# Kernel tuning notes

Hardware: AMD Instinct MI355X
Metric: run time of the kernel (lower is better)

Reference implementation:

```python
import jax, jax.numpy as jnp
import numpy as np

NUM_HEADS = 32
NUM_KV_GROUPS = 8


def _rope(x, cos, sin):
    # x: [B, H, S, hd]; cos/sin: [S_max, hd]
    S, hd = x.shape[2], x.shape[3]
    x1, x2 = x[..., : hd // 2], x[..., hd // 2 :]
    rotated = jnp.concatenate((-x2, x1), axis=-1)
    c = cos[:S][None, None]
    s = sin[:S][None, None]
    return (x * c + rotated * s).astype(x.dtype)


def setup_inputs() -> dict:
    key = jax.random.key(0)
    ks = jax.random.split(key, 8)
    B, S, D = 2, 2048, 2048
    H, G = NUM_HEADS, NUM_KV_GROUPS
    hd = D // H
    scale = 1.0 / np.sqrt(D)
    return {
        "inputs": jax.random.normal(ks[0], (B, S, D), jnp.float32),
        "mask": jnp.zeros((S, S), jnp.bool_),  # note: original masked_fill is not in-place -> mask unused
        "cos": jax.random.uniform(ks[1], (S, hd), jnp.float32),
        "sin": jax.random.uniform(ks[2], (S, hd), jnp.float32),
        "Wq": jax.random.normal(ks[3], (D, H * hd), jnp.float32) * scale,
        "Wk": jax.random.normal(ks[4], (D, G * hd), jnp.float32) * scale,
        "Wv": jax.random.normal(ks[5], (D, G * hd), jnp.float32) * scale,
        "Wo": jax.random.normal(ks[6], (H * hd, H * hd), jnp.float32) * scale,
    }


def reference(inputs, mask, cos, sin, Wq, Wk, Wv, Wo):
    B, S, D = inputs.shape
    H, G = NUM_HEADS, NUM_KV_GROUPS
    hd = Wq.shape[1] // H
    group_size = H // G

    q = (inputs @ Wq).reshape(B, S, H, hd).transpose(0, 2, 1, 3)  # [B,H,S,hd]
    k = (inputs @ Wk).reshape(B, S, G, hd).transpose(0, 2, 1, 3)  # [B,G,S,hd]
    v = (inputs @ Wv).reshape(B, S, G, hd).transpose(0, 2, 1, 3)

    q = _rope(q, cos, sin)
    k = _rope(k, cos, sin)

    k = jnp.repeat(k, group_size, axis=1)  # [B,H,S,hd]
    v = jnp.repeat(v, group_size, axis=1)

    scores = jnp.einsum("bhqd,bhkd->bhqk", q, k)
    # NOTE: original uses non-inplace masked_fill whose result is discarded,
    # so faithfully NO mask is applied.
    attn = jax.nn.softmax(scores / jnp.sqrt(jnp.float32(hd)).astype(scores.dtype), axis=-1)
    ctx = jnp.einsum("bhqk,bhkd->bhqd", attn, v)
    ctx = ctx.transpose(0, 2, 1, 3).reshape(B, S, H * hd)
    return ctx @ Wo
```

## Files before the change

kernel.cpp:

```cpp
#include <hip/hip_runtime.h>
#include <stdint.h>

typedef __attribute__((ext_vector_type(8))) short short8;
typedef __attribute__((ext_vector_type(4))) short short4v;
typedef __attribute__((ext_vector_type(4))) float float4v;
typedef __attribute__((ext_vector_type(2))) unsigned uint2v;

__device__ __forceinline__ float bf2f(short s) {
  union { unsigned u; float f; } x;
  x.u = ((unsigned)(unsigned short)s) << 16;
  return x.f;
}
__device__ __forceinline__ short f2bf(float f) {
  union { float f; unsigned u; } x;
  x.f = f;
  unsigned r = x.u + 0x7fffu + ((x.u >> 16) & 1u);
  return (short)(r >> 16);
}
__device__ __forceinline__ float fexp2(float x) {
#if __has_builtin(__builtin_amdgcn_exp2f)
  return __builtin_amdgcn_exp2f(x);
#else
  float r;
  asm("v_exp_f32 %0, %1" : "=v"(r) : "v"(x));
  return r;
#endif
}
__device__ __forceinline__ void glds16(const void* g, void* l) {
  __builtin_amdgcn_global_load_lds(
      (const __attribute__((address_space(1))) void*)g,
      (__attribute__((address_space(3))) void*)l, 16, 0, 0);
}
__device__ __forceinline__ void sbar() {
  __builtin_amdgcn_sched_barrier(0);
  __builtin_amdgcn_s_barrier();
  __builtin_amdgcn_sched_barrier(0);
}

__global__ __launch_bounds__(256) void f32_to_bf16(const float* __restrict__ s,
                                                   short* __restrict__ d) {
  const long i = ((long)blockIdx.x * 256 + threadIdx.x) * 8;
  const float4v a = *(const float4v*)&s[i];
  const float4v b = *(const float4v*)&s[i + 4];
  short8 v;
#pragma unroll
  for (int e = 0; e < 4; ++e) { v[e] = f2bf(a[e]); v[e + 4] = f2bf(b[e]); }
  *(short8*)&d[i] = v;
}

__device__ __forceinline__ void transpose_tile(
    const float* __restrict__ src, short* __restrict__ dst, int R, int C,
    int r0, int c0) {
  __shared__ short t[64 * 72];
  const int tid = threadIdx.x;
#pragma unroll
  for (int r = 0; r < 2; ++r) {
    int c = r * 256 + tid;
    int row = c >> 3, col8 = (c & 7) * 8;
    const float4v a = *(const float4v*)&src[(long)(r0 + row) * C + c0 + col8];
    const float4v b = *(const float4v*)&src[(long)(r0 + row) * C + c0 + col8 + 4];
    short8 v;
#pragma unroll
    for (int e = 0; e < 4; ++e) { v[e] = f2bf(a[e]); v[e + 4] = f2bf(b[e]); }
    *(short8*)&t[row * 72 + col8] = v;
  }
  __syncthreads();
#pragma unroll
  for (int r = 0; r < 2; ++r) {
    int c = r * 256 + tid;
    int orow = c >> 3, ocol8 = (c & 7) * 8;
    short8 w;
#pragma unroll
    for (int e = 0; e < 8; ++e) w[e] = t[(ocol8 + e) * 72 + orow];
    *(short8*)&dst[(long)(c0 + orow) * R + r0 + ocol8] = w;
  }
}

__global__ __launch_bounds__(256) void transpose_f2b(
    const float* __restrict__ src, short* __restrict__ dst, int R, int C) {
  transpose_tile(src, dst, R, C, blockIdx.y * 64, blockIdx.x * 64);
}

__global__ __launch_bounds__(256) void wtrans3(
    const float* __restrict__ Wq, const float* __restrict__ Wk,
    const float* __restrict__ Wv, short* __restrict__ WT) {
  const int z = blockIdx.z;
  const float* src = z == 0 ? Wq : (z == 1 ? Wk : Wv);
  const int C = z == 0 ? 2048 : 512;
  if (blockIdx.x * 64 >= C) return;
  short* dst = WT + (z == 0 ? 0 : (z == 1 ? 2048 * 2048 : 2560 * 2048));
  transpose_tile(src, dst, 2048, C, blockIdx.y * 64, blockIdx.x * 64);
}

__global__ __launch_bounds__(256) void vtrans(const short* __restrict__ Y,
                                              short* __restrict__ Vt,
                                              int ld, int col0) {
  const int bg = blockIdx.y;
  const int b = bg >> 3, gk = bg & 7;
  const int s0 = blockIdx.x * 64;
  __shared__ short t[64 * 72];
  const int tid = threadIdx.x;
#pragma unroll
  for (int r = 0; r < 2; ++r) {
    int c = r * 256 + tid;
    int row = c >> 3, col8 = (c & 7) * 8;
    short8 v = *(const short8*)&Y[(long)(b * 2048 + s0 + row) * ld + col0 + gk * 64 + col8];
    *(short8*)&t[row * 72 + col8] = v;
  }
  __syncthreads();
#pragma unroll
  for (int r = 0; r < 2; ++r) {
    int c = r * 256 + tid;
    int d = c >> 3, s8 = (c & 7) * 8;
    short8 w;
#pragma unroll
    for (int e = 0; e < 8; ++e) w[e] = t[(s8 + e) * 72 + d];
    *(short8*)&Vt[((long)bg * 64 + d) * 2048 + s0 + s8] = w;
  }
}

__global__ __launch_bounds__(256) void rope_kernel(
    const short* __restrict__ Y, const float* __restrict__ cosp,
    const float* __restrict__ sinp, short* __restrict__ out,
    int NH, int lgNH, int ld, int col0, float scale) {
  const long tid = (long)blockIdx.x * 256 + threadIdx.x;
  const int d = (int)(tid & 31);
  const long t1 = tid >> 5;
  const int h = (int)(t1 & (NH - 1));
  const long t2 = t1 >> lgNH;
  const int s = (int)(t2 & 2047);
  const int b = (int)(t2 >> 11);
  const long ib = (long)(b * 2048 + s) * ld + col0 + h * 64 + d;
  const float x1 = bf2f(Y[ib]);
  const float x2 = bf2f(Y[ib + 32]);
  const float c1 = cosp[s * 64 + d];
  const float c2 = cosp[s * 64 + d + 32];
  const float s1 = sinp[s * 64 + d];
  const float s2 = sinp[s * 64 + d + 32];
  const long ob = ((long)(b * NH + h) * 2048 + s) * 64 + d;
  out[ob] = f2bf((x1 * c1 - x2 * s1) * scale);
  out[ob + 32] = f2bf((x2 * c2 + x1 * s2) * scale);
}

template <typename OutT>
__global__ __launch_bounds__(512, 2) void gemm256(
    const short* __restrict__ A, const short* __restrict__ BT,
    OutT* __restrict__ C, int M, int N, int K) {
  (void)M;
  __shared__ short As[2][16384];
  __shared__ short Bs[2][16384];
  const int tid = threadIdx.x;
  const int w = tid >> 6, lane = tid & 63;
  const int g = lane >> 4, lr = lane & 15;
  const int wm = w >> 2, wn = w & 3;
  const int m0 = blockIdx.y << 8, n0 = blockIdx.x << 8;

  const int r0 = tid >> 3;
  const int scol = ((tid & 7) << 3) ^ (((r0 >> 2) & 1) << 4);
  const long aoff = (long)(m0 + r0) * K + scol;
  const long boff = (long)(n0 + r0) * K + scol;

  const int swz = ((lr >> 2) & 1) << 4;
  const int acol0 = (g << 3) ^ swz;
  const int acol1 = (32 + (g << 3)) ^ swz;
  const int abase = (wm * 128 + lr) * 64;
  const int bbase = (wn * 64 + lr) * 64;

  float4v acc[8][4];
#pragma unroll
  for (int i = 0; i < 8; ++i)
#pragma unroll
    for (int j = 0; j < 4; ++j) acc[i][j] = (float4v)0.f;

#define STAGE_A(l, buf, kg)                                          \
  glds16(A + aoff + (long)(l) * 64 * K + (kg),                       \
         &As[(buf)][(l) * 4096 + w * 512])
#define STAGE_B(l, buf, kg)                                          \
  glds16(BT + boff + (long)(l) * 64 * K + (kg),                      \
         &Bs[(buf)][(l) * 4096 + w * 512])

  const int NT = K >> 6;
#pragma unroll
  for (int l = 0; l < 4; ++l) { STAGE_A(l, 0, 0); STAGE_B(l, 0, 0); }
#pragma unroll
  for (int l = 0; l < 4; ++l) { STAGE_A(l, 1, 64); STAGE_B(l, 1, 64); }
  asm volatile("s_waitcnt vmcnt(8)" ::: "memory");
  sbar();

  short8 aR[4][2], bR0[2][2], bR1[2][2];

#define LDA(MH, ASB)                                                       \
  _Pragma("unroll") for (int i = 0; i < 4; ++i) {                          \
    aR[i][0] = *(const short8*)&ASB[abase + ((MH)*4 + i) * 1024 + acol0];  \
    aR[i][1] = *(const short8*)&ASB[abase + ((MH)*4 + i) * 1024 + acol1];  \
  }
#define LDB(NH, BSB, BR)                                                   \
  _Pragma("unroll") for (int j = 0; j < 2; ++j) {                          \
    BR[j][0] = *(const short8*)&BSB[bbase + ((NH)*2 + j) * 1024 + acol0];  \
    BR[j][1] = *(const short8*)&BSB[bbase + ((NH)*2 + j) * 1024 + acol1];  \
  }
#define MMA_Q(MH, NH, BR)                                                  \
  __builtin_amdgcn_s_setprio(1);                                           \
  _Pragma("unroll") for (int kk = 0; kk < 2; ++kk)                         \
  _Pragma("unroll") for (int i = 0; i < 4; ++i)                            \
  _Pragma("unroll") for (int j = 0; j < 2; ++j)                            \
    acc[(MH)*4 + i][(NH)*2 + j] = __builtin_amdgcn_mfma_f32_16x16x32_bf16( \
        aR[i][kk], BR[j][kk], acc[(MH)*4 + i][(NH)*2 + j], 0, 0, 0);       \
  __builtin_amdgcn_s_setprio(0);

  for (int t = 0; t < NT; ++t) {
    const short* const Asb = As[t & 1];
    const short* const Bsb = Bs[t & 1];
    const long kg = (long)(t + 2) << 6;
    const bool pre = (t + 2) < NT;

    LDA(0, Asb);
    LDB(0, Bsb, bR0);
    sbar();
    MMA_Q(0, 0, bR0);
    sbar();
    LDB(1, Bsb, bR1);
    if (pre) { STAGE_A(0, t & 1, kg); STAGE_A(2, t & 1, kg); }
    sbar();
    MMA_Q(0, 1, bR1);
    sbar();
    LDA(1, Asb);
    if (pre) {
      STAGE_B(0, t & 1, kg); STAGE_B(1, t & 1, kg);
      STAGE_B(2, t & 1, kg); STAGE_B(3, t & 1, kg);
    }
    sbar();
    MMA_Q(1, 1, bR1);
    sbar();
    if (pre) { STAGE_A(1, t & 1, kg); STAGE_A(3, t & 1, kg); }
    sbar();
    MMA_Q(1, 0, bR0);
    __builtin_amdgcn_sched_barrier(0);
    if (pre) { asm volatile("s_waitcnt vmcnt(8)" ::: "memory"); }
    else     { asm volatile("s_waitcnt vmcnt(0)" ::: "memory"); }
    sbar();
  }

#pragma unroll
  for (int i = 0; i < 8; ++i)
#pragma unroll
    for (int j = 0; j < 4; ++j)
#pragma unroll
      for (int t4 = 0; t4 < 4; ++t4) {
        const int r = m0 + wm * 128 + i * 16 + g * 4 + t4;
        const int cc = n0 + wn * 64 + j * 16 + lr;
        const float v = acc[i][j][t4];
        if constexpr (sizeof(OutT) == 2)
          C[(long)r * N + cc] = f2bf(v);
        else
          C[(long)r * N + cc] = v;
      }
#undef STAGE_A
#undef STAGE_B
#undef LDA
#undef LDB
#undef MMA_Q
}

__global__ __launch_bounds__(512, 2) void attn_kernel(
    const short* __restrict__ Qr, const short* __restrict__ Kr,
    const short* __restrict__ Vt, short* __restrict__ Ctx) {
  constexpr int S = 2048;
  const int bh = blockIdx.y;
  const int b = bh >> 5, h = bh & 31;
  const int gk = h >> 2;
  const int q0 = blockIdx.x << 7;
  const int tid = threadIdx.x;
  const int w = tid >> 6, lane = tid & 63;
  const int g = lane >> 4, lr = lane & 15;
  const int b8 = lr & 7;
  const int qrow = w * 16 + lr;

  __shared__ short Ks[128 * 64];
  __shared__ short Vs[64 * 128];
  __shared__ short Ps[128 * 128];

  const short* Qb = Qr + (long)(b * 32 + h) * S * 64;
  const short* KbIt = Kr + (long)(b * 8 + gk) * S * 64;
  const short* VbIt = Vt + (long)(b * 8 + gk) * 64 * S;

  const int ko0 = lr * 64 + ((0 + g) ^ b8) * 8;
  const int ko1 = lr * 64 + ((4 + g) ^ b8) * 8;
  const int jv0 = g ^ b8;
  const int vo0 = lr * 128 + jv0 * 8;
  const int vo1 = lr * 128 + (jv0 ^ 4) * 8;
  int pr[4], pw[8];
#pragma unroll
  for (int ks = 0; ks < 4; ++ks) pr[ks] = qrow * 128 + ((4 * ks + g) ^ b8) * 8;
#pragma unroll
  for (int i = 0; i < 8; ++i)
    pw[i] = qrow * 128 + ((2 * i + (g >> 1)) ^ b8) * 8 + (g & 1) * 4;

  long koff[2], voff[2];
#pragma unroll
  for (int r = 0; r < 2; ++r) {
    const int c = r * 512 + w * 64 + lane;
    const int kv = c >> 3, slot = c & 7;
    koff[r] = (long)kv * 64 + (slot ^ (kv & 7)) * 8;
    const int dd = c >> 4, s16 = c & 15;
    voff[r] = (long)dd * S + ((s16 & 8) | ((s16 & 7) ^ (dd & 7))) * 8;
  }

  short8 qf[2];
  qf[0] = *(const short8*)&Qb[(long)(q0 + qrow) * 64 + g * 8];
  qf[1] = *(const short8*)&Qb[(long)(q0 + qrow) * 64 + 32 + g * 8];

  const short8 ones = (short8)(short)0x3F80;
  float4v lacc = (float4v)0.f;
  float4v oacc[4];
#pragma unroll
  for (int di = 0; di < 4; ++di) oacc[di] = (float4v)0.f;

  for (int it = 0; it < 16; ++it) {
#pragma unroll
    for (int r = 0; r < 2; ++r) {
      const int cb = r * 512 + w * 64;
      glds16(KbIt + koff[r], Ks + cb * 8);
      glds16(VbIt + voff[r], Vs + cb * 8);
    }
    __syncthreads();

    float4v sacc[8];
#pragma unroll
    for (int i = 0; i < 8; ++i) sacc[i] = (float4v)0.f;
#pragma unroll
    for (int i = 0; i < 8; ++i) {
      const short8 a0 = *(const short8*)&Ks[ko0 + i * 1024];
      sacc[i] = __builtin_amdgcn_mfma_f32_16x16x32_bf16(a0, qf[0], sacc[i], 0, 0, 0);
    }
#pragma unroll
    for (int i = 0; i < 8; ++i) {
      const short8 a1 = *(const short8*)&Ks[ko1 + i * 1024];
      sacc[i] = __builtin_amdgcn_mfma_f32_16x16x32_bf16(a1, qf[1], sacc[i], 0, 0, 0);
    }

#pragma unroll
    for (int i = 0; i < 8; ++i) {
      union { float f; unsigned u; } a0, a1, a2, a3;
      a0.f = fexp2(sacc[i][0]);
      a1.f = fexp2(sacc[i][1]);
      a2.f = fexp2(sacc[i][2]);
      a3.f = fexp2(sacc[i][3]);
      const unsigned d0 = __builtin_amdgcn_perm(a1.u + 0x8000u, a0.u + 0x8000u, 0x07060302u);
      const unsigned d1 = __builtin_amdgcn_perm(a3.u + 0x8000u, a2.u + 0x8000u, 0x07060302u);
      *(uint2v*)&Ps[pw[i]] = (uint2v){d0, d1};
    }

#pragma unroll
    for (int ks = 0; ks < 4; ++ks) {
      const short8 pf = *(const short8*)&Ps[pr[ks]];
      const int vbase = (ks & 1) ? vo1 : vo0;
      lacc = __builtin_amdgcn_mfma_f32_16x16x32_bf16(ones, pf, lacc, 0, 0, 0);
#pragma unroll
      for (int di = 0; di < 4; ++di) {
        const short8 vf = *(const short8*)&Vs[vbase + di * 2048 + (ks >> 1) * 64];
        oacc[di] = __builtin_amdgcn_mfma_f32_16x16x32_bf16(vf, pf, oacc[di], 0, 0, 0);
      }
    }
    __syncthreads();
    KbIt += 128 * 64;
    VbIt += 128;
  }

  const float inv = 1.f / lacc[0];

  const int q = q0 + qrow;
#pragma unroll
  for (int di = 0; di < 4; ++di) {
    short4v o;
#pragma unroll
    for (int t = 0; t < 4; ++t) o[t] = f2bf(oacc[di][t] * inv);
    *(short4v*)&Ctx[(long)(b * S + q) * 2048 + h * 64 + di * 16 + g * 4] = o;
  }
}

extern "C" void kernel_launch(void* const* d_in, const int* in_sizes, int n_in,
                              void* d_out, int out_size, void* d_ws, size_t ws_size,
                              hipStream_t stream) {
  (void)in_sizes; (void)n_in; (void)out_size; (void)ws_size;
  const float* X    = (const float*)d_in[0];
  const float* cosp = (const float*)d_in[2];
  const float* sinp = (const float*)d_in[3];
  const float* Wq   = (const float*)d_in[4];
  const float* Wk   = (const float*)d_in[5];
  const float* Wv   = (const float*)d_in[6];
  const float* Wo   = (const float*)d_in[7];
  float* out = (float*)d_out;
  char* ws = (char*)d_ws;

  short* Xb = (short*)(ws + 0);
  short* WT = (short*)(ws + 16777216);
  short* Y  = (short*)(ws + 29360128);
  short* Qr = (short*)(ws + 54525952);
  short* Kr = (short*)(ws + 71303168);
  short* Vt = (short*)(ws + 75497472);

  f32_to_bf16<<<4096, 256, 0, stream>>>(X, Xb);
  wtrans3<<<dim3(32, 32, 3), 256, 0, stream>>>(Wq, Wk, Wv, WT);

  gemm256<short><<<dim3(12, 16), 512, 0, stream>>>(Xb, WT, Y, 4096, 3072, 2048);

  transpose_f2b<<<dim3(32, 32), 256, 0, stream>>>(Wo, WT, 2048, 2048);

  rope_kernel<<<16384, 256, 0, stream>>>(Y, cosp, sinp, Qr, 32, 5, 3072, 0, 0.18033688011112043f);
  rope_kernel<<<4096, 256, 0, stream>>>(Y, cosp, sinp, Kr, 8, 3, 3072, 2048, 1.0f);
  vtrans<<<dim3(32, 16), 256, 0, stream>>>(Y, Vt, 3072, 2560);

  attn_kernel<<<dim3(16, 64), 512, 0, stream>>>(Qr, Kr, Vt, Y);

  gemm256<float><<<dim3(8, 16), 512, 0, stream>>>(Y, WT, out, 4096, 2048, 2048);
}
```

Measured before the change: 386.4 us.

## Double-buffer attention K/V tiles and remap GEMM block order with wider swizzle

The attention kernel switches from 128-key single-buffered tiles to 64-key double-buffered tiles. It prefetches the next K/V tile with async global-to-LDS loads and uses explicit vmcnt waits so loads overlap compute. This shrinks shared memory and raises the occupancy hint to 6 blocks per SM. The GEMM also remaps block IDs across 8 groups (an XCD-aware ordering) and extends the LDS XOR swizzle by one bit to reduce bank conflicts. Risks include register pressure under the higher launch bound, plus more iterations and barriers per tile.

New measurement: 379.9 us. No clear change (-1.7%).

```diff
diff --git a/kernel.cpp b/kernel.cpp
--- a/kernel.cpp
+++ b/kernel.cpp
@@ -153,14 +153,20 @@
   const int w = tid >> 6, lane = tid & 63;
   const int g = lane >> 4, lr = lane & 15;
   const int wm = w >> 2, wn = w & 3;
-  const int m0 = blockIdx.y << 8, n0 = blockIdx.x << 8;
+
+  const int nbx = gridDim.x;
+  const int nwg = nbx * gridDim.y;
+  const int bid = blockIdx.y * nbx + blockIdx.x;
+  const int cpx = nwg >> 3;
+  const int nbid = (bid & 7) * cpx + (bid >> 3);
+  const int m0 = (nbid / nbx) << 8, n0 = (nbid % nbx) << 8;
 
   const int r0 = tid >> 3;
-  const int scol = ((tid & 7) << 3) ^ (((r0 >> 2) & 1) << 4);
+  const int scol = ((tid & 7) << 3) ^ (((r0 >> 2) & 1) << 4) ^ (((r0 >> 3) & 1) << 5);
   const long aoff = (long)(m0 + r0) * K + scol;
   const long boff = (long)(n0 + r0) * K + scol;
 
-  const int swz = ((lr >> 2) & 1) << 4;
+  const int swz = (((lr >> 2) & 1) << 4) | (((lr >> 3) & 1) << 5);
   const int acol0 = (g << 3) ^ swz;
   const int acol1 = (32 + (g << 3)) ^ swz;
   const int abase = (wm * 128 + lr) * 64;
@@ -262,10 +268,11 @@
 #undef MMA_Q
 }
 
-__global__ __launch_bounds__(512, 2) void attn_kernel(
+__global__ __launch_bounds__(512, 6) void attn_kernel(
     const short* __restrict__ Qr, const short* __restrict__ Kr,
     const short* __restrict__ Vt, short* __restrict__ Ctx) {
   constexpr int S = 2048;
+  constexpr int NIT = 32;
   const int bh = blockIdx.y;
   const int b = bh >> 5, h = bh & 31;
   const int gk = h >> 2;
@@ -276,35 +283,29 @@
   const int b8 = lr & 7;
   const int qrow = w * 16 + lr;
 
-  __shared__ short Ks[128 * 64];
-  __shared__ short Vs[64 * 128];
-  __shared__ short Ps[128 * 128];
+  __shared__ short Ks[2][64 * 64];
+  __shared__ short Vs[2][64 * 64];
+  __shared__ short Ps[128 * 64];
 
   const short* Qb = Qr + (long)(b * 32 + h) * S * 64;
-  const short* KbIt = Kr + (long)(b * 8 + gk) * S * 64;
-  const short* VbIt = Vt + (long)(b * 8 + gk) * 64 * S;
+  const short* Kb = Kr + (long)(b * 8 + gk) * S * 64;
+  const short* Vb = Vt + (long)(b * 8 + gk) * 64 * S;
 
   const int ko0 = lr * 64 + ((0 + g) ^ b8) * 8;
   const int ko1 = lr * 64 + ((4 + g) ^ b8) * 8;
-  const int jv0 = g ^ b8;
-  const int vo0 = lr * 128 + jv0 * 8;
-  const int vo1 = lr * 128 + (jv0 ^ 4) * 8;
-  int pr[4], pw[8];
-#pragma unroll
-  for (int ks = 0; ks < 4; ++ks) pr[ks] = qrow * 128 + ((4 * ks + g) ^ b8) * 8;
-#pragma unroll
-  for (int i = 0; i < 8; ++i)
-    pw[i] = qrow * 128 + ((2 * i + (g >> 1)) ^ b8) * 8 + (g & 1) * 4;
-
-  long koff[2], voff[2];
-#pragma unroll
-  for (int r = 0; r < 2; ++r) {
-    const int c = r * 512 + w * 64 + lane;
-    const int kv = c >> 3, slot = c & 7;
-    koff[r] = (long)kv * 64 + (slot ^ (kv & 7)) * 8;
-    const int dd = c >> 4, s16 = c & 15;
-    voff[r] = (long)dd * S + ((s16 & 8) | ((s16 & 7) ^ (dd & 7))) * 8;
-  }
+  int vo[2], pr[2], pw[4];
+#pragma unroll
+  for (int ks = 0; ks < 2; ++ks) {
+    vo[ks] = lr * 64 + ((ks * 4 + g) ^ b8) * 8;
+    pr[ks] = qrow * 64 + ((ks * 4 + g) ^ b8) * 8;
+  }
+#pragma unroll
+  for (int i = 0; i < 4; ++i)
+    pw[i] = qrow * 64 + ((2 * i + (g >> 1)) ^ b8) * 8 + (g & 1) * 4;
+
+  const int srow = tid >> 3, sl = tid & 7;
+  const long koff = (long)srow * 64 + (sl ^ (srow & 7)) * 8;
+  const long voff = (long)srow * S + (sl ^ (srow & 7)) * 8;
 
   short8 qf[2];
   qf[0] = *(const short8*)&Qb[(long)(q0 + qrow) * 64 + g * 8];
@@ -316,31 +317,38 @@
 #pragma unroll
   for (int di = 0; di < 4; ++di) oacc[di] = (float4v)0.f;
 
-  for (int it = 0; it < 16; ++it) {
-#pragma unroll
-    for (int r = 0; r < 2; ++r) {
-      const int cb = r * 512 + w * 64;
-      glds16(KbIt + koff[r], Ks + cb * 8);
-      glds16(VbIt + voff[r], Vs + cb * 8);
-    }
-    __syncthreads();
-
-    float4v sacc[8];
-#pragma unroll
-    for (int i = 0; i < 8; ++i) sacc[i] = (float4v)0.f;
-#pragma unroll
-    for (int i = 0; i < 8; ++i) {
-      const short8 a0 = *(const short8*)&Ks[ko0 + i * 1024];
+  glds16(Kb + koff, &Ks[0][w * 512]);
+  glds16(Vb + voff, &Vs[0][w * 512]);
+
+  for (int it = 0; it < NIT; ++it) {
+    const int buf = it & 1;
+    if (it + 1 < NIT) {
+      glds16(Kb + (long)(it + 1) * 64 * 64 + koff, &Ks[buf ^ 1][w * 512]);
+      glds16(Vb + (it + 1) * 64 + voff, &Vs[buf ^ 1][w * 512]);
+      __builtin_amdgcn_sched_barrier(0);
+      asm volatile("s_waitcnt vmcnt(2)" ::: "memory");
+    } else {
+      __builtin_amdgcn_sched_barrier(0);
+      asm volatile("s_waitcnt vmcnt(0)" ::: "memory");
+    }
+    sbar();
+
+    float4v sacc[4];
+#pragma unroll
+    for (int i = 0; i < 4; ++i) sacc[i] = (float4v)0.f;
+#pragma unroll
+    for (int i = 0; i < 4; ++i) {
+      const short8 a0 = *(const short8*)&Ks[buf][ko0 + i * 1024];
       sacc[i] = __builtin_amdgcn_mfma_f32_16x16x32_bf16(a0, qf[0], sacc[i], 0, 0, 0);
     }
 #pragma unroll
-    for (int i = 0; i < 8; ++i) {
-      const short8 a1 = *(const short8*)&Ks[ko1 + i * 1024];
+    for (int i = 0; i < 4; ++i) {
+      const short8 a1 = *(const short8*)&Ks[buf][ko1 + i * 1024];
       sacc[i] = __builtin_amdgcn_mfma_f32_16x16x32_bf16(a1, qf[1], sacc[i], 0, 0, 0);
     }
 
 #pragma unroll
-    for (int i = 0; i < 8; ++i) {
+    for (int i = 0; i < 4; ++i) {
       union { float f; unsigned u; } a0, a1, a2, a3;
       a0.f = fexp2(sacc[i][0]);
       a1.f = fexp2(sacc[i][1]);
@@ -352,19 +360,16 @@
     }
 
 #pragma unroll
-    for (int ks = 0; ks < 4; ++ks) {
+    for (int ks = 0; ks < 2; ++ks) {
       const short8 pf = *(const short8*)&Ps[pr[ks]];
-      const int vbase = (ks & 1) ? vo1 : vo0;
       lacc = __builtin_amdgcn_mfma_f32_16x16x32_bf16(ones, pf, lacc, 0, 0, 0);
 #pragma unroll
       for (int di = 0; di < 4; ++di) {
-        const short8 vf = *(const short8*)&Vs[vbase + di * 2048 + (ks >> 1) * 64];
+        const short8 vf = *(const short8*)&Vs[buf][vo[ks] + di * 1024];
         oacc[di] = __builtin_amdgcn_mfma_f32_16x16x32_bf16(vf, pf, oacc[di], 0, 0, 0);
       }
     }
-    __syncthreads();
-    KbIt += 128 * 64;
-    VbIt += 128;
+    sbar();
   }
 
   const float inv = 1.f / lacc[0];
```
